# Kernel optimization log

Measured on AMD Instinct MI355X. Metric: run time of the kernel, lower is better.

The kernel has to match this reference:

```python
import jax, jax.numpy as jnp
import numpy as np

D_MODEL = 2048
EXPAND = 2
D_INNER = D_MODEL * EXPAND            # 4096
HEAD_DIM = 64
NHEADS = D_INNER // HEAD_DIM          # 64
D_STATE = 128
NGROUPS = 1
D_CONV = 4
CHUNK = 256
CONV_DIM = D_INNER + 2 * NGROUPS * D_STATE      # 4352
D_IN_PROJ = 2 * D_INNER + 2 * NGROUPS * D_STATE + NHEADS  # 8512
EPS = 1e-5


def segsum(x):
    # x: [..., T] -> [..., T, T] lower-triangular segment sums (incl. diagonal)
    T = x.shape[-1]
    xc = jnp.cumsum(x, axis=-1)
    diff = xc[..., :, None] - xc[..., None, :]
    mask = jnp.tril(jnp.ones((T, T), dtype=bool))
    return jnp.where(mask, diff, -jnp.inf)


def causal_conv1d(x, w, b):
    # x: [B,L,C]  depthwise causal conv, kernel K; w: [C,K], b: [C]
    K = w.shape[1]
    L = x.shape[1]
    xp = jnp.pad(x, ((0, 0), (K - 1, 0), (0, 0)))
    y = b[None, None, :]
    for k in range(K):
        y = y + xp[:, k:k + L, :] * w[None, None, :, k]
    return jax.nn.silu(y)


def ssd_chunked(x, dt, A, B, C, Dskip):
    # x:[b,l,h,p] dt:[b,l,h] A:[h] B,C:[b,l,g,n] Dskip:[h]
    b, l, h, p = x.shape
    g, n = B.shape[2], B.shape[3]
    c = l // CHUNK
    xc = x.reshape(b, c, CHUNK, h, p)
    dtc = dt.reshape(b, c, CHUNK, h)
    Bh = jnp.repeat(B.reshape(b, c, CHUNK, g, n), h // g, axis=3)  # [b,c,s,h,n]
    Ch = jnp.repeat(C.reshape(b, c, CHUNK, g, n), h // g, axis=3)
    dA = dtc * A[None, None, None, :]            # [b,c,s,h]
    dAc = jnp.moveaxis(dA, 3, 1)                 # [b,h,c,s]
    A_cumsum = jnp.cumsum(dAc, axis=-1)          # [b,h,c,s]
    Lmat = jnp.exp(segsum(dAc))                  # [b,h,c,s,s]
    # intra-chunk (diagonal blocks)
    Y_diag = jnp.einsum('bclhn,bcshn,bhcls,bcsh,bcshp->bclhp', Ch, Bh, Lmat, dtc, xc)
    # per-chunk final states
    decay_states = jnp.exp(A_cumsum[..., -1:] - A_cumsum)   # [b,h,c,s]
    states = jnp.einsum('bclhn,bhcl,bclh,bclhp->bchpn', Bh, decay_states, dtc, xc)
    states = jnp.concatenate([jnp.zeros_like(states[:, :1]), states], axis=1)  # [b,c+1,h,p,n]
    # inter-chunk recurrence
    chunk_sums = jnp.pad(A_cumsum[..., -1], ((0, 0), (0, 0), (1, 0)))  # [b,h,c+1]
    decay_chunk = jnp.exp(segsum(chunk_sums))    # [b,h,c+1,c+1]
    new_states = jnp.einsum('bhzc,bchpn->bzhpn', decay_chunk, states)
    states_prev = new_states[:, :-1]             # state entering each chunk
    state_decay_out = jnp.exp(A_cumsum)          # [b,h,c,s]
    Y_off = jnp.einsum('bclhn,bchpn,bhcl->bclhp', Ch, states_prev, state_decay_out)
    Y = (Y_diag + Y_off).reshape(b, l, h, p) + x * Dskip[None, None, :, None]
    return Y


def gated_rmsnorm(y, z, w):
    # norm_before_gate=False: rmsnorm(y * silu(z)) * w, grouped (g=NGROUPS)
    x = y * jax.nn.silu(z)
    gs = D_INNER // NGROUPS
    xg = x.reshape(x.shape[:-1] + (NGROUPS, gs))
    var = jnp.mean(xg * xg, axis=-1, keepdims=True)
    xg = xg * jax.lax.rsqrt(var + EPS)
    return xg.reshape(x.shape) * w[None, None, :]


def setup_inputs() -> dict:
    key = jax.random.key(0)
    ks = jax.random.split(key, 9)
    B, L = 2, 2048
    return {
        'hidden_states': jax.random.normal(ks[0], (B, L, D_MODEL), jnp.float32),
        'W_in': jax.random.normal(ks[1], (D_MODEL, D_IN_PROJ), jnp.float32) * 0.02,
        'conv_w': jax.random.normal(ks[2], (CONV_DIM, D_CONV), jnp.float32) * 0.2,
        'conv_b': jax.random.normal(ks[3], (CONV_DIM,), jnp.float32) * 0.02,
        'A': -jnp.exp(jax.random.normal(ks[4], (NHEADS,), jnp.float32) * 0.5),
        'D': jax.random.normal(ks[5], (NHEADS,), jnp.float32) * 0.5,
        'dt_bias': jax.random.normal(ks[6], (NHEADS,), jnp.float32) * 0.5,
        'norm_w': jnp.ones((D_INNER,), jnp.float32) + jax.random.normal(ks[7], (D_INNER,), jnp.float32) * 0.02,
        'W_out': jax.random.normal(ks[8], (D_INNER, D_MODEL), jnp.float32) * 0.02,
    }


def reference(hidden_states, W_in, conv_w, conv_b, A, D, dt_bias, norm_w, W_out):
    b, l, _ = hidden_states.shape
    zxbcdt = hidden_states @ W_in  # [b,l,d_in_proj]
    z = zxbcdt[..., :D_INNER]
    xbc = zxbcdt[..., D_INNER:D_INNER + CONV_DIM]
    dt = zxbcdt[..., D_INNER + CONV_DIM:]
    xbc = causal_conv1d(xbc, conv_w, conv_b)
    x = xbc[..., :D_INNER].reshape(b, l, NHEADS, HEAD_DIM)
    Bs = xbc[..., D_INNER:D_INNER + NGROUPS * D_STATE].reshape(b, l, NGROUPS, D_STATE)
    Cs = xbc[..., D_INNER + NGROUPS * D_STATE:].reshape(b, l, NGROUPS, D_STATE)
    dt = jax.nn.softplus(dt + dt_bias[None, None, :])
    y = ssd_chunked(x, dt, A, Bs, Cs, D).reshape(b, l, D_INNER)
    y = gated_rmsnorm(y, z, norm_w)
    return y @ W_out
```

## Files before the change

kernel.cpp:

```cpp
#include <hip/hip_runtime.h>
#include <hip/hip_bf16.h>
#include <math.h>

#define D_MODEL   2048
#define D_INNER   4096
#define NHEADS    64
#define HEAD_DIM  64
#define D_STATE   128
#define CHUNK     256
#define CONV_DIM  (D_INNER + 2*D_STATE)
#define D_IN_PROJ (2*D_INNER + 2*D_STATE + NHEADS)
#define LD_ZX     8704
#define DT_OFF    (2*D_INNER + 2*D_STATE)
#define BATCH     2
#define SEQ       2048
#define NCHUNK    (SEQ/CHUNK)
#define EPS_RMS   1e-5f
#define MROWS     4096
#define TSTRIDE   ((size_t)MROWS * 512)

typedef unsigned short u16;
typedef __attribute__((ext_vector_type(8))) unsigned short u16x8;
typedef __attribute__((ext_vector_type(4))) unsigned short u16x4;
typedef __attribute__((ext_vector_type(8))) short bf16x8;
typedef __attribute__((ext_vector_type(4))) float f32x4;

__device__ __forceinline__ float us2f(u16 u){
    union { unsigned int i; float f; } c; c.i = ((unsigned int)u) << 16; return c.f;
}
__device__ __forceinline__ u16 f2us(float f){
    union { float f; unsigned int i; } c; c.f = f;
    unsigned int r = c.i + 0x7FFFu + ((c.i >> 16) & 1u);
    return (u16)(r >> 16);
}
__device__ __forceinline__ float siluf(float x){ return x / (1.f + expf(-x)); }

__device__ __forceinline__ void gload_lds16(const void* g, void* l) {
    __builtin_amdgcn_global_load_lds((const __attribute__((address_space(1))) void*)g,
                                     (__attribute__((address_space(3))) void*)l, 16, 0, 0);
}

#define VMCNT(n) asm volatile("s_waitcnt vmcnt(" #n ")" ::: "memory")

__device__ __forceinline__ void stage_half(const u16* __restrict__ g, size_t ldk,
                                           u16* ldsbase, int w, int lane)
{
    #pragma unroll
    for (int cc = 0; cc < 2; cc++) {
        int cb = cc * 512 + w * 64;
        int ci = cb + lane;
        int sc = ci ^ ((ci >> 3) & 7);
        gload_lds16(&g[(size_t)(sc >> 3) * ldk + (sc & 7) * 8], ldsbase + cb * 8);
    }
}

__global__ __launch_bounds__(256)
void cvt_bf16(const float* __restrict__ in, u16* __restrict__ out, int n4)
{
    int i = blockIdx.x * 256 + threadIdx.x;
    if (i >= n4) return;
    float4 v = *(const float4*)&in[(size_t)i * 4];
    u16x4 o; o[0]=f2us(v.x); o[1]=f2us(v.y); o[2]=f2us(v.z); o[3]=f2us(v.w);
    *(u16x4*)&out[(size_t)i * 4] = o;
}

__global__ __launch_bounds__(256)
void add_tmp_bf16(float* __restrict__ out, const u16* __restrict__ tmp, int n8)
{
    int i = blockIdx.x * 256 + threadIdx.x;
    if (i >= n8) return;
    u16x8 b = *(const u16x8*)&tmp[(size_t)i * 8];
    float* o = &out[(size_t)i * 8];
    float4 a0 = *(const float4*)&o[0];
    float4 a1 = *(const float4*)&o[4];
    *(float4*)&o[0] = make_float4(a0.x+us2f(b[0]), a0.y+us2f(b[1]), a0.z+us2f(b[2]), a0.w+us2f(b[3]));
    *(float4*)&o[4] = make_float4(a1.x+us2f(b[4]), a1.y+us2f(b[5]), a1.z+us2f(b[6]), a1.w+us2f(b[7]));
}

__global__ __launch_bounds__(256)
void transpose_cvt(const float* __restrict__ in, u16* __restrict__ out, int K, int N)
{
    __shared__ u16 tile[64][65];
    int k0 = blockIdx.x * 64;
    int n0 = blockIdx.y * 64;
    int t = threadIdx.x;
    #pragma unroll
    for (int q = 0; q < 16; q++) {
        int lin = q * 256 + t;
        int r = lin >> 6, c = lin & 63;
        int n = n0 + c;
        float v = (n < N) ? in[(size_t)(k0 + r) * N + n] : 0.f;
        tile[r][c] = f2us(v);
    }
    __syncthreads();
    #pragma unroll
    for (int q = 0; q < 4; q++) {
        int lin = q * 256 + t;
        int r = lin >> 4, cg = lin & 15;
        u16x4 v;
        #pragma unroll
        for (int e = 0; e < 4; e++) v[e] = tile[cg*4 + e][r];
        *(u16x4*)&out[(size_t)(n0 + r) * K + k0 + cg*4] = v;
    }
}

template<typename TC, bool KSPLIT>
__global__ __launch_bounds__(512, 1)
void gemm_8ph(const u16* __restrict__ Ag, const u16* __restrict__ Btg,
              TC* __restrict__ Cg, u16* __restrict__ Cg2,
              int M, int N, int Kext, int ldk, int ldc)
{
    __shared__ u16 smA[2][2][8192];
    __shared__ u16 smB[2][2][8192];
    const int tid = threadIdx.x;
    const int lane = tid & 63, w = tid >> 6;
    const int wm = w >> 2, wn = w & 3;
    const int lr = lane & 15, kh = lane >> 4;
    const int swz = (lr & 7) << 3;

    int orig = blockIdx.x;
    int ntile = gridDim.x;
    int kidx = 0;
    if constexpr (KSPLIT) { kidx = orig & 1; orig >>= 1; ntile >>= 1; }

    const int nbx = N >> 8;
    const int qq = ntile >> 3, r8 = ntile & 7;
    const int xcd = orig & 7, loc = orig >> 3;
    const int wgid = (xcd < r8 ? xcd*(qq+1) : r8*(qq+1) + (xcd-r8)*qq) + loc;
    const int m0 = (wgid / nbx) * 256;
    const int n0 = (wgid % nbx) * 256;

    if constexpr (KSPLIT) {
        Ag  += (size_t)kidx * Kext;
        Btg += (size_t)kidx * Kext;
    }
    const int NT = Kext >> 6;

    f32x4 acc[8][4];
    #pragma unroll
    for (int i = 0; i < 8; i++)
        #pragma unroll
        for (int j = 0; j < 4; j++) acc[i][j] = (f32x4){0.f,0.f,0.f,0.f};

    stage_half(&Ag [(size_t)(m0      ) * ldk      ], ldk, &smA[0][0][0], w, lane);
    stage_half(&Ag [(size_t)(m0 + 128) * ldk      ], ldk, &smA[0][1][0], w, lane);
    stage_half(&Btg[(size_t)(n0      ) * ldk      ], ldk, &smB[0][0][0], w, lane);
    stage_half(&Btg[(size_t)(n0 + 128) * ldk      ], ldk, &smB[0][1][0], w, lane);
    stage_half(&Ag [(size_t)(m0      ) * ldk + 64 ], ldk, &smA[1][0][0], w, lane);
    stage_half(&Btg[(size_t)(n0      ) * ldk + 64 ], ldk, &smB[1][0][0], w, lane);
    stage_half(&Btg[(size_t)(n0 + 128) * ldk + 64 ], ldk, &smB[1][1][0], w, lane);
    VMCNT(6);
    __builtin_amdgcn_s_barrier();

    for (int t = 0; t < NT; ++t) {
        const int d = t & 1;
        const u16* As = &smA[d][wm][0];
        const u16* Bs = &smB[d][wn >> 1][0];
        const int rb = (wn & 1) * 64;

        bf16x8 aF[4][2], bLo[2][2], bHi[2][2];

        #pragma unroll
        for (int i = 0; i < 4; i++)
            #pragma unroll
            for (int ks = 0; ks < 2; ks++)
                aF[i][ks] = *(const bf16x8*)&As[(i*16 + lr)*64 + ((ks*32 + kh*8) ^ swz)];
        #pragma unroll
        for (int j = 0; j < 2; j++)
            #pragma unroll
            for (int ks = 0; ks < 2; ks++)
                bLo[j][ks] = *(const bf16x8*)&Bs[(rb + j*16 + lr)*64 + ((ks*32 + kh*8) ^ swz)];
        if (t + 1 < NT)
            stage_half(&Ag[(size_t)(m0 + 128) * ldk + (t+1)*64], ldk, &smA[d^1][1][0], w, lane);
        __builtin_amdgcn_s_barrier();
        __builtin_amdgcn_s_setprio(1);
        #pragma unroll
        for (int i = 0; i < 4; i++)
            #pragma unroll
            for (int j = 0; j < 2; j++)
                #pragma unroll
                for (int ks = 0; ks < 2; ks++)
                    acc[i][j] = __builtin_amdgcn_mfma_f32_16x16x32_bf16(aF[i][ks], bLo[j][ks], acc[i][j], 0, 0, 0);
        __builtin_amdgcn_s_setprio(0);
        __builtin_amdgcn_s_barrier();

        #pragma unroll
        for (int j = 0; j < 2; j++)
            #pragma unroll
            for (int ks = 0; ks < 2; ks++)
                bHi[j][ks] = *(const bf16x8*)&Bs[(rb + (2+j)*16 + lr)*64 + ((ks*32 + kh*8) ^ swz)];
        __builtin_amdgcn_s_barrier();
        __builtin_amdgcn_s_setprio(1);
        #pragma unroll
        for (int i = 0; i < 4; i++)
            #pragma unroll
            for (int j = 0; j < 2; j++)
                #pragma unroll
                for (int ks = 0; ks < 2; ks++)
                    acc[i][2+j] = __builtin_amdgcn_mfma_f32_16x16x32_bf16(aF[i][ks], bHi[j][ks], acc[i][2+j], 0, 0, 0);
        __builtin_amdgcn_s_setprio(0);
        __builtin_amdgcn_s_barrier();

        #pragma unroll
        for (int i = 0; i < 4; i++)
            #pragma unroll
            for (int ks = 0; ks < 2; ks++)
                aF[i][ks] = *(const bf16x8*)&As[(64 + i*16 + lr)*64 + ((ks*32 + kh*8) ^ swz)];
        if (t + 2 < NT)
            stage_half(&Btg[(size_t)(n0) * ldk + (t+2)*64], ldk, &smB[d][0][0], w, lane);
        __builtin_amdgcn_s_barrier();
        __builtin_amdgcn_s_setprio(1);
        #pragma unroll
        for (int i = 0; i < 4; i++)
            #pragma unroll
            for (int j = 0; j < 2; j++)
                #pragma unroll
                for (int ks = 0; ks < 2; ks++)
                    acc[4+i][j] = __builtin_amdgcn_mfma_f32_16x16x32_bf16(aF[i][ks], bLo[j][ks], acc[4+i][j], 0, 0, 0);
        __builtin_amdgcn_s_setprio(0);
        __builtin_amdgcn_s_barrier();

        if (t + 2 < NT) {
            stage_half(&Btg[(size_t)(n0 + 128) * ldk + (t+2)*64], ldk, &smB[d][1][0], w, lane);
            stage_half(&Ag [(size_t)(m0      ) * ldk + (t+2)*64], ldk, &smA[d][0][0], w, lane);
        }
        __builtin_amdgcn_s_barrier();
        __builtin_amdgcn_s_setprio(1);
        #pragma unroll
        for (int i = 0; i < 4; i++)
            #pragma unroll
            for (int j = 0; j < 2; j++)
                #pragma unroll
                for (int ks = 0; ks < 2; ks++)
                    acc[4+i][2+j] = __builtin_amdgcn_mfma_f32_16x16x32_bf16(aF[i][ks], bHi[j][ks], acc[4+i][2+j], 0, 0, 0);
        __builtin_amdgcn_s_setprio(0);
        if (t < NT - 2)       { VMCNT(6); }
        else if (t == NT - 2) { VMCNT(0); }
        __builtin_amdgcn_s_barrier();
    }

    #pragma unroll
    for (int mf = 0; mf < 8; mf++) {
        #pragma unroll
        for (int nf = 0; nf < 4; nf++) {
            int r = m0 + wm*128 + mf*16 + kh*4;
            int cidx = n0 + wn*64 + nf*16 + lr;
            #pragma unroll
            for (int q = 0; q < 4; q++) {
                if (KSPLIT && kidx) {
                    Cg2[(size_t)(r+q)*ldc + cidx] = f2us(acc[mf][nf][q]);
                } else if constexpr (sizeof(TC) == 4) {
                    Cg[(size_t)(r+q)*ldc + cidx] = acc[mf][nf][q];
                } else {
                    Cg[(size_t)(r+q)*ldc + cidx] = f2us(acc[mf][nf][q]);
                }
            }
        }
    }
}

__global__ __launch_bounds__(256)
void gemm_tail_ks4(const u16* __restrict__ A, const u16* __restrict__ Bt,
                   float* __restrict__ Cp, int M, int ldk)
{
    __shared__ u16 Asm[128][32];
    __shared__ u16 Bsm[128][32];
    const int t = threadIdx.x;
    const int lane = t & 63, w = t >> 6;
    const int wr = w >> 1, wc = w & 1;
    const int lr = lane & 15, kh = lane >> 4;

    const int bid = blockIdx.x;
    const int kidx = bid & 3, tile = bid >> 2;
    const int m0 = (tile >> 2) * 128;
    const int n0 = (tile & 3) * 128;

    const u16* Ak = A  + kidx * 512;
    const u16* Bk = Bt + kidx * 512;
    float* C = Cp + (size_t)kidx * TSTRIDE;

    f32x4 acc[4][4];
    #pragma unroll
    for (int i = 0; i < 4; i++)
        #pragma unroll
        for (int j = 0; j < 4; j++) acc[i][j] = (f32x4){0.f,0.f,0.f,0.f};

    for (int k0 = 0; k0 < 512; k0 += 32) {
        #pragma unroll
        for (int i = 0; i < 2; i++) {
            int cb = i * 256 + w * 64;
            int chunk = cb + lane;
            int row = chunk >> 2, kb = chunk & 3;
            gload_lds16(&Ak[(size_t)(m0 + row) * ldk + k0 + kb * 8], &Asm[0][0] + cb * 8);
            gload_lds16(&Bk[(size_t)(n0 + row) * ldk + k0 + kb * 8], &Bsm[0][0] + cb * 8);
        }
        __syncthreads();
        bf16x8 af[4], bf[4];
        #pragma unroll
        for (int i = 0; i < 4; i++)
            af[i] = *(const bf16x8*)&Asm[wr*64 + i*16 + lr][kh*8];
        #pragma unroll
        for (int j = 0; j < 4; j++)
            bf[j] = *(const bf16x8*)&Bsm[wc*64 + j*16 + lr][kh*8];
        #pragma unroll
        for (int i = 0; i < 4; i++)
            #pragma unroll
            for (int j = 0; j < 4; j++)
                acc[i][j] = __builtin_amdgcn_mfma_f32_16x16x32_bf16(af[i], bf[j], acc[i][j], 0, 0, 0);
        __syncthreads();
    }
    #pragma unroll
    for (int i = 0; i < 4; i++) {
        #pragma unroll
        for (int j = 0; j < 4; j++) {
            int r = m0 + wr*64 + i*16 + kh*4;
            int cidx = n0 + wc*64 + j*16 + lr;
            #pragma unroll
            for (int q = 0; q < 4; q++)
                C[(size_t)(r+q)*512 + cidx] = acc[i][j][q];
        }
    }
}

__global__ __launch_bounds__(256)
void conv_silu(const u16* __restrict__ zx, const float* __restrict__ tailp,
               const float* __restrict__ cw, const float* __restrict__ cb,
               u16* __restrict__ xconv, u16* __restrict__ Bbuf, u16* __restrict__ Cbuf)
{
    int idx = blockIdx.x * 256 + threadIdx.x;
    int cg = idx % (CONV_DIM / 8);
    int r  = idx / (CONV_DIM / 8);
    int c0 = cg * 8;
    int l  = r & (SEQ - 1);

    float y[8];
    {
        float4 b0 = *(const float4*)&cb[c0];
        float4 b1 = *(const float4*)&cb[c0 + 4];
        y[0]=b0.x; y[1]=b0.y; y[2]=b0.z; y[3]=b0.w;
        y[4]=b1.x; y[5]=b1.y; y[6]=b1.z; y[7]=b1.w;
    }
    float cwf[8][4];
    #pragma unroll
    for (int e = 0; e < 8; e++) {
        float4 v = *(const float4*)&cw[(c0 + e) * 4];
        cwf[e][0]=v.x; cwf[e][1]=v.y; cwf[e][2]=v.z; cwf[e][3]=v.w;
    }
    if (c0 < D_INNER) {
        #pragma unroll
        for (int k = 0; k < 4; k++) {
            if (l + k - 3 >= 0) {
                u16x8 v = *(const u16x8*)&zx[(size_t)(r + k - 3) * LD_ZX + D_INNER + c0];
                #pragma unroll
                for (int e = 0; e < 8; e++) y[e] += us2f(v[e]) * cwf[e][k];
            }
        }
    } else {
        int tc = c0 - D_INNER;
        #pragma unroll
        for (int k = 0; k < 4; k++) {
            if (l + k - 3 >= 0) {
                const float* tb = &tailp[(size_t)(r + k - 3) * 512 + tc];
                #pragma unroll
                for (int e = 0; e < 8; e++) {
                    float s = tb[e] + tb[TSTRIDE + e] + tb[2*TSTRIDE + e] + tb[3*TSTRIDE + e];
                    y[e] += s * cwf[e][k];
                }
            }
        }
    }
    u16x8 o;
    #pragma unroll
    for (int e = 0; e < 8; e++) {
        float s = y[e] / (1.f + expf(-y[e]));
        o[e] = f2us(s);
    }
    if (c0 < D_INNER)                *(u16x8*)&xconv[(size_t)r * D_INNER + c0] = o;
    else if (c0 < D_INNER + D_STATE) *(u16x8*)&Bbuf[(size_t)r * D_STATE + (c0 - D_INNER)] = o;
    else                             *(u16x8*)&Cbuf[(size_t)r * D_STATE + (c0 - D_INNER - D_STATE)] = o;
}

__global__ __launch_bounds__(256)
void dt_acs(const float* __restrict__ tailp, const float* __restrict__ Aparam,
            const float* __restrict__ dt_bias, float* __restrict__ dtT,
            float* __restrict__ Acs)
{
    __shared__ float sb[CHUNK];
    int blk = blockIdx.x;
    int c = blk & 7, h = (blk >> 3) & 63, b = blk >> 9;
    int t = threadIdx.x;
    int lg = c * CHUNK + t;
    int row = b * SEQ + lg;
    const float* tb = &tailp[(size_t)row * 512 + 256 + h];
    float x = tb[0] + tb[TSTRIDE] + tb[2*TSTRIDE] + tb[3*TSTRIDE];
    x += dt_bias[h];
    float dt = (x > 20.f) ? x : log1pf(expf(x));
    float v = dt * Aparam[h];
    sb[t] = v; __syncthreads();
    #pragma unroll
    for (int off = 1; off < 256; off <<= 1) {
        float add = (t >= off) ? sb[t - off] : 0.f;
        __syncthreads();
        v += add; sb[t] = v;
        __syncthreads();
    }
    int o = (b * NHEADS + h) * SEQ + lg;
    dtT[o] = dt;
    Acs[o] = v;
}

__global__ __launch_bounds__(256)
void chunk_states_mfma(const u16* __restrict__ xconv, const u16* __restrict__ Bbuf,
                       const float* __restrict__ dtT, const float* __restrict__ Acs,
                       u16* __restrict__ states)
{
    __shared__ u16 Btsh[128][72];
    __shared__ u16 xtsh[64][72];
    __shared__ float acs_sh[CHUNK];
    __shared__ float dt_sh[CHUNK];

    const int blk = blockIdx.x;
    const int h = blk & 63, c = (blk >> 6) & 7, b = blk >> 9;
    const int t = threadIdx.x;
    const int lane = t & 63, w = t >> 6;
    const int wr = w >> 1, wc = w & 1;
    const int lr = lane & 15, kh = lane >> 4;
    const int bh = b * NHEADS + h;
    const size_t rowbase = (size_t)(b * SEQ + c * CHUNK);

    acs_sh[t] = Acs[(size_t)bh * SEQ + c * CHUNK + t];
    dt_sh[t]  = dtT[(size_t)bh * SEQ + c * CHUNK + t];
    __syncthreads();
    const float acs_last = acs_sh[CHUNK - 1];

    f32x4 acc[4][2];
    #pragma unroll
    for (int j = 0; j < 4; j++)
        #pragma unroll
        for (int i = 0; i < 2; i++) acc[j][i] = (f32x4){0.f,0.f,0.f,0.f};

    for (int lt = 0; lt < 4; lt++) {
        __syncthreads();
        const int s = t & 63;
        const int sg = lt * 64 + s;
        const float wgt = dt_sh[sg] * expf(acs_last - acs_sh[sg]);
        {
            int ng = (t >> 6) * 32;
            const u16* src = &Bbuf[(rowbase + sg) * D_STATE + ng];
            #pragma unroll
            for (int q = 0; q < 4; q++) {
                u16x8 v = *(const u16x8*)&src[q * 8];
                #pragma unroll
                for (int e = 0; e < 8; e++)
                    Btsh[ng + q*8 + e][s] = v[e];
            }
        }
        {
            int pg = (t >> 6) * 16;
            const u16* src = &xconv[(rowbase + sg) * D_INNER + h * HEAD_DIM + pg];
            u16x8 v0 = *(const u16x8*)&src[0];
            u16x8 v1 = *(const u16x8*)&src[8];
            #pragma unroll
            for (int e = 0; e < 8; e++) {
                xtsh[pg + e][s]     = f2us(us2f(v0[e]) * wgt);
                xtsh[pg + 8 + e][s] = f2us(us2f(v1[e]) * wgt);
            }
        }
        __syncthreads();
        #pragma unroll
        for (int kk = 0; kk < 2; kk++) {
            bf16x8 xf[2], bf[4];
            #pragma unroll
            for (int i = 0; i < 2; i++)
                xf[i] = *(const bf16x8*)&xtsh[wr*32 + i*16 + lr][kk*32 + kh*8];
            #pragma unroll
            for (int j = 0; j < 4; j++)
                bf[j] = *(const bf16x8*)&Btsh[wc*64 + j*16 + lr][kk*32 + kh*8];
            #pragma unroll
            for (int j = 0; j < 4; j++)
                #pragma unroll
                for (int i = 0; i < 2; i++)
                    acc[j][i] = __builtin_amdgcn_mfma_f32_16x16x32_bf16(bf[j], xf[i], acc[j][i], 0, 0, 0);
        }
    }
    size_t base = ((size_t)((b*NCHUNK + c)*NHEADS + h)) * (HEAD_DIM * D_STATE);
    #pragma unroll
    for (int j = 0; j < 4; j++) {
        #pragma unroll
        for (int i = 0; i < 2; i++) {
            int p = wr*32 + i*16 + lr;
            int n = wc*64 + j*16 + kh*4;
            u16x4 o;
            #pragma unroll
            for (int q = 0; q < 4; q++) o[q] = f2us(acc[j][i][q]);
            *(u16x4*)&states[base + (size_t)p * D_STATE + n] = o;
        }
    }
}

__global__ __launch_bounds__(256)
void state_recurrence(u16* __restrict__ states, const float* __restrict__ Acs)
{
    int idx = blockIdx.x * 256 + threadIdx.x;
    int n8 = idx & 15;
    int p  = (idx >> 4) & 63;
    int bh = idx >> 10;
    int b = bh >> 6, h = bh & 63;
    float E[8];
    #pragma unroll
    for (int e = 0; e < 8; e++) E[e] = 0.f;
    for (int c = 0; c < NCHUNK; c++) {
        size_t off = ((size_t)((b*NCHUNK + c)*NHEADS + h)) * 8192 + (size_t)p * 128 + n8 * 8;
        u16x8 sv = *(const u16x8*)&states[off];
        u16x8 ev;
        #pragma unroll
        for (int e = 0; e < 8; e++) ev[e] = f2us(E[e]);
        *(u16x8*)&states[off] = ev;
        float g = expf(Acs[(size_t)(b*NHEADS + h) * SEQ + c*CHUNK + 255]);
        #pragma unroll
        for (int e = 0; e < 8; e++) E[e] = g * E[e] + us2f(sv[e]);
    }
}

__global__ __launch_bounds__(256, 1)
void chunk_output_mfma(const u16* __restrict__ xconv, const u16* __restrict__ Bbuf,
                       const u16* __restrict__ Cbuf, const float* __restrict__ dtT,
                       const float* __restrict__ Acs, const u16* __restrict__ states,
                       const float* __restrict__ Dparam, u16* __restrict__ Y)
{
    __shared__ u16 Bsm[64][136];
    __shared__ u16 xt[64][72];
    __shared__ u16 Pt[4][64][72];
    __shared__ float acs_sh[CHUNK];
    __shared__ float dt_sh[CHUNK];

    const int blk = blockIdx.x;
    const int h = blk & 63, c = (blk >> 6) & 7, b = blk >> 9;
    const int t = threadIdx.x;
    const int lane = t & 63, w = t >> 6;
    const int lr = lane & 15, kh = lane >> 4;
    const int bh = b * NHEADS + h;
    const size_t rowbase = (size_t)(b * SEQ + c * CHUNK);

    acs_sh[t] = Acs[(size_t)bh * SEQ + c * CHUNK + t];
    dt_sh[t]  = dtT[(size_t)bh * SEQ + c * CHUNK + t];

    bf16x8 af[4][4];
    #pragma unroll
    for (int i = 0; i < 4; i++)
        #pragma unroll
        for (int kk = 0; kk < 4; kk++)
            af[i][kk] = *(const bf16x8*)&Cbuf[(rowbase + w*64 + i*16 + lr) * D_STATE + kk*32 + kh*8];

    {
        int p = t >> 2, ng = (t & 3) * 32;
        const u16* src = &states[((size_t)((b*NCHUNK + c)*NHEADS + h)) * 8192 + (size_t)p * 128 + ng];
        #pragma unroll
        for (int q = 0; q < 4; q++)
            *(u16x8*)&Bsm[p][ng + q*8] = *(const u16x8*)&src[q*8];
    }
    __syncthreads();
    float acs_l[4], el[4];
    #pragma unroll
    for (int i = 0; i < 4; i++) { acs_l[i] = acs_sh[w*64 + i*16 + lr]; el[i] = expf(acs_l[i]); }

    f32x4 yacc[4][4];
    #pragma unroll
    for (int j = 0; j < 4; j++)
        #pragma unroll
        for (int i = 0; i < 4; i++) yacc[j][i] = (f32x4){0.f,0.f,0.f,0.f};
    #pragma unroll
    for (int kk = 0; kk < 4; kk++) {
        bf16x8 pvA[4];
        #pragma unroll
        for (int j = 0; j < 4; j++)
            pvA[j] = *(const bf16x8*)&Bsm[j*16 + lr][kk*32 + kh*8];
        #pragma unroll
        for (int j = 0; j < 4; j++)
            #pragma unroll
            for (int i = 0; i < 4; i++)
                yacc[j][i] = __builtin_amdgcn_mfma_f32_16x16x32_bf16(pvA[j], af[i][kk], yacc[j][i], 0, 0, 0);
    }
    #pragma unroll
    for (int j = 0; j < 4; j++)
        #pragma unroll
        for (int i = 0; i < 4; i++)
            #pragma unroll
            for (int q = 0; q < 4; q++)
                yacc[j][i][q] *= el[i];

    for (int st = 0; st < 4; st++) {
        __syncthreads();
        {
            int sr = t >> 2, cg = (t & 3) * 32;
            const u16* src = &Bbuf[(rowbase + st*64 + sr) * D_STATE + cg];
            #pragma unroll
            for (int q = 0; q < 4; q++)
                *(u16x8*)&Bsm[sr][cg + q*8] = *(const u16x8*)&src[q*8];
        }
        {
            int s = t & 63, pg = t >> 6;
            const u16* src = &xconv[(rowbase + st*64 + s) * D_INNER + h*HEAD_DIM + pg*16];
            u16x8 v0 = *(const u16x8*)&src[0];
            u16x8 v1 = *(const u16x8*)&src[8];
            #pragma unroll
            for (int q = 0; q < 8; q++) { xt[pg*16 + q][s] = v0[q]; xt[pg*16 + 8 + q][s] = v1[q]; }
        }
        __syncthreads();
        if (st > w) continue;

        f32x4 sacc[4][4];
        #pragma unroll
        for (int js = 0; js < 4; js++)
            #pragma unroll
            for (int i = 0; i < 4; i++) sacc[js][i] = (f32x4){0.f,0.f,0.f,0.f};
        #pragma unroll
        for (int kk = 0; kk < 4; kk++) {
            bf16x8 bA[4];
            #pragma unroll
            for (int js = 0; js < 4; js++)
                bA[js] = *(const bf16x8*)&Bsm[js*16 + lr][kk*32 + kh*8];
            #pragma unroll
            for (int js = 0; js < 4; js++)
                #pragma unroll
                for (int i = 0; i < 4; i++)
                    sacc[js][i] = __builtin_amdgcn_mfma_f32_16x16x32_bf16(bA[js], af[i][kk], sacc[js][i], 0, 0, 0);
        }
        #pragma unroll
        for (int js = 0; js < 4; js++) {
            int s0 = st*64 + js*16;
            float as0 = acs_sh[s0];
            int sgq = s0 + kh*4;
            float eneg[4];
            #pragma unroll
            for (int q = 0; q < 4; q++)
                eneg[q] = expf(fminf(as0 - acs_sh[sgq + q], 60.f)) * dt_sh[sgq + q];
            #pragma unroll
            for (int i = 0; i < 4; i++) {
                float eladj = expf(acs_l[i] - as0);
                int lg = w*64 + i*16 + lr;
                u16x4 pv;
                #pragma unroll
                for (int q = 0; q < 4; q++) {
                    float fac = (sgq + q <= lg) ? eladj * eneg[q] : 0.f;
                    pv[q] = f2us(sacc[js][i][q] * fac);
                }
                *(u16x4*)&Pt[w][i*16 + lr][js*16 + kh*4] = pv;
            }
        }
        #pragma unroll
        for (int kk2 = 0; kk2 < 2; kk2++) {
            bf16x8 xA[4], pB[4];
            #pragma unroll
            for (int j = 0; j < 4; j++)
                xA[j] = *(const bf16x8*)&xt[j*16 + lr][kk2*32 + kh*8];
            #pragma unroll
            for (int i = 0; i < 4; i++)
                pB[i] = *(const bf16x8*)&Pt[w][i*16 + lr][kk2*32 + kh*8];
            #pragma unroll
            for (int j = 0; j < 4; j++)
                #pragma unroll
                for (int i = 0; i < 4; i++)
                    yacc[j][i] = __builtin_amdgcn_mfma_f32_16x16x32_bf16(xA[j], pB[i], yacc[j][i], 0, 0, 0);
        }
    }

    float Dh = Dparam[h];
    #pragma unroll
    for (int i = 0; i < 4; i++) {
        #pragma unroll
        for (int j = 0; j < 4; j++) {
            size_t o = (rowbase + w*64 + i*16 + lr) * D_INNER + h*HEAD_DIM + j*16 + kh*4;
            u16x4 xv = *(const u16x4*)&xconv[o];
            u16x4 ov;
            #pragma unroll
            for (int q = 0; q < 4; q++)
                ov[q] = f2us(yacc[j][i][q] + Dh * us2f(xv[q]));
            *(u16x4*)&Y[o] = ov;
        }
    }
}

__global__ __launch_bounds__(256)
void gated_rmsnorm_k(u16* __restrict__ Y, const u16* __restrict__ zx,
                     const float* __restrict__ nw)
{
    __shared__ float xs[D_INNER];
    __shared__ float red[8];
    int row = blockIdx.x;
    int t = threadIdx.x;
    float ss = 0.f;
    for (int i = t*8; i < D_INNER; i += 2048) {
        u16x8 yv = *(const u16x8*)&Y[(size_t)row * D_INNER + i];
        u16x8 zv = *(const u16x8*)&zx[(size_t)row * LD_ZX + i];
        #pragma unroll
        for (int q = 0; q < 8; q++) {
            float x = us2f(yv[q]) * siluf(us2f(zv[q]));
            xs[i + q] = x;
            ss += x * x;
        }
    }
    #pragma unroll
    for (int off = 32; off > 0; off >>= 1) ss += __shfl_down(ss, off);
    int wid = t >> 6, lane = t & 63;
    if (lane == 0) red[wid] = ss;
    __syncthreads();
    if (t == 0) {
        float tot = red[0] + red[1] + red[2] + red[3];
        red[0] = rsqrtf(tot / (float)D_INNER + EPS_RMS);
    }
    __syncthreads();
    float sc = red[0];
    for (int i = t*8; i < D_INNER; i += 2048) {
        u16x8 o;
        #pragma unroll
        for (int q = 0; q < 8; q++) o[q] = f2us(xs[i + q] * sc * nw[i + q]);
        *(u16x8*)&Y[(size_t)row * D_INNER + i] = o;
    }
}

__global__ void ws_fail_k(float* out, float mb){ out[threadIdx.x] = mb; }

extern "C" void kernel_launch(void* const* d_in, const int* in_sizes, int n_in,
                              void* d_out, int out_size, void* d_ws, size_t ws_size,
                              hipStream_t stream)
{
    const float* hidden  = (const float*)d_in[0];
    const float* W_in    = (const float*)d_in[1];
    const float* conv_w  = (const float*)d_in[2];
    const float* conv_b  = (const float*)d_in[3];
    const float* Aparam  = (const float*)d_in[4];
    const float* Dparam  = (const float*)d_in[5];
    const float* dt_bias = (const float*)d_in[6];
    const float* norm_w  = (const float*)d_in[7];
    const float* W_out   = (const float*)d_in[8];
    float* out = (float*)d_out;

    const int M = BATCH * SEQ;

    size_t off = 0;
    char* wsb = (char*)d_ws;
    u16*   zx     = (u16*)  (wsb + off); off += (size_t)M * LD_ZX * 2;
    u16*   xconv  = (u16*)  (wsb + off); off += (size_t)M * D_INNER * 2;
    u16*   Bbuf   = (u16*)  (wsb + off); off += (size_t)M * D_STATE * 2;
    u16*   Cbuf   = (u16*)  (wsb + off); off += (size_t)M * D_STATE * 2;
    float* dtT    = (float*)(wsb + off); off += (size_t)BATCH * NHEADS * SEQ * 4;
    float* Acs    = (float*)(wsb + off); off += (size_t)BATCH * NHEADS * SEQ * 4;
    u16*   states = (u16*)  (wsb + off); off += (size_t)BATCH * NCHUNK * NHEADS * HEAD_DIM * D_STATE * 2;
    u16*   Ybuf   = (u16*)  (wsb + off); off += (size_t)M * D_INNER * 2;
    u16*   hbf    = (u16*)  (wsb + off); off += (size_t)M * D_MODEL * 2;
    u16*   WtIn   = (u16*)  (wsb + off); off += (size_t)LD_ZX * D_MODEL * 2;
    u16*   WtOut  = (u16*)  (wsb + off); off += (size_t)D_MODEL * D_INNER * 2;
    float* tailp  = (float*)(wsb + off); off += 4 * TSTRIDE * 4;
    u16*   tmpf   = (u16*)zx;

    if (off > ws_size) {
        ws_fail_k<<<1, 64, 0, stream>>>(out, (float)(ws_size >> 20));
        return;
    }

    cvt_bf16<<<(M * D_MODEL / 4 + 255) / 256, 256, 0, stream>>>(hidden, hbf, M * D_MODEL / 4);
    transpose_cvt<<<dim3(D_MODEL/64, LD_ZX/64), 256, 0, stream>>>(W_in, WtIn, D_MODEL, D_IN_PROJ);
    transpose_cvt<<<dim3(D_INNER/64, D_MODEL/64), 256, 0, stream>>>(W_out, WtOut, D_INNER, D_MODEL);

    gemm_8ph<u16, false><<<(8192/256) * (M/256), 512, 0, stream>>>(
        hbf, WtIn, zx, nullptr, M, 8192, D_MODEL, D_MODEL, LD_ZX);
    gemm_tail_ks4<<<512, 256, 0, stream>>>(hbf, WtIn + (size_t)8192 * D_MODEL, tailp, M, D_MODEL);

    conv_silu<<<(M * CONV_DIM / 8) / 256, 256, 0, stream>>>(zx, tailp, conv_w, conv_b, xconv, Bbuf, Cbuf);
    dt_acs<<<BATCH * NHEADS * NCHUNK, 256, 0, stream>>>(tailp, Aparam, dt_bias, dtT, Acs);
    chunk_states_mfma<<<BATCH * NCHUNK * NHEADS, 256, 0, stream>>>(xconv, Bbuf, dtT, Acs, states);
    state_recurrence<<<(BATCH * NHEADS * 64 * 16) / 256, 256, 0, stream>>>(states, Acs);
    chunk_output_mfma<<<BATCH * NCHUNK * NHEADS, 256, 0, stream>>>(xconv, Bbuf, Cbuf, dtT, Acs, states, Dparam, Ybuf);
    gated_rmsnorm_k<<<M, 256, 0, stream>>>(Ybuf, zx, norm_w);

    gemm_8ph<float, true><<<2 * (D_MODEL/256) * (M/256), 512, 0, stream>>>(
        Ybuf, WtOut, out, tmpf, M, D_MODEL, D_INNER/2, D_INNER, D_MODEL);
    add_tmp_bf16<<<(M * D_MODEL / 8 + 255) / 256, 256, 0, stream>>>(out, tmpf, M * D_MODEL / 8);
}
```

Measured before the change: 476.8 us.

## Precompute head-shared C·Bᵀ per chunk and write both split-K halves as bf16

With one group, the per-chunk C·Bᵀ score matrix is the same for every head. A new kernel computes the lower-triangular 64x64 blocks of it once per (batch, chunk) and stores them as bf16. The chunk output kernel then reads those scores instead of recomputing them with MFMA for each of the 64 heads. This removes redundant matmul work and B staging, at the cost of extra global reads and bf16 rounding of the scores. Separately, the split-K out-projection now writes both halves as bf16 temporaries that a final kernel sums, instead of writing fp32 output and then reading it back to add the second half.

```diff
diff --git a/kernel.cpp b/kernel.cpp
--- a/kernel.cpp
+++ b/kernel.cpp
@@ -65,16 +65,18 @@
 }
 
 __global__ __launch_bounds__(256)
-void add_tmp_bf16(float* __restrict__ out, const u16* __restrict__ tmp, int n8)
+void add2_bf16(float* __restrict__ out, const u16* __restrict__ t0,
+               const u16* __restrict__ t1, int n8)
 {
     int i = blockIdx.x * 256 + threadIdx.x;
     if (i >= n8) return;
-    u16x8 b = *(const u16x8*)&tmp[(size_t)i * 8];
+    u16x8 a = *(const u16x8*)&t0[(size_t)i * 8];
+    u16x8 b = *(const u16x8*)&t1[(size_t)i * 8];
     float* o = &out[(size_t)i * 8];
-    float4 a0 = *(const float4*)&o[0];
-    float4 a1 = *(const float4*)&o[4];
-    *(float4*)&o[0] = make_float4(a0.x+us2f(b[0]), a0.y+us2f(b[1]), a0.z+us2f(b[2]), a0.w+us2f(b[3]));
-    *(float4*)&o[4] = make_float4(a1.x+us2f(b[4]), a1.y+us2f(b[5]), a1.z+us2f(b[6]), a1.w+us2f(b[7]));
+    *(float4*)&o[0] = make_float4(us2f(a[0])+us2f(b[0]), us2f(a[1])+us2f(b[1]),
+                                  us2f(a[2])+us2f(b[2]), us2f(a[3])+us2f(b[3]));
+    *(float4*)&o[4] = make_float4(us2f(a[4])+us2f(b[4]), us2f(a[5])+us2f(b[5]),
+                                  us2f(a[6])+us2f(b[6]), us2f(a[7])+us2f(b[7]));
 }
 
 __global__ __launch_bounds__(256)
@@ -133,6 +135,7 @@
     if constexpr (KSPLIT) {
         Ag  += (size_t)kidx * Kext;
         Btg += (size_t)kidx * Kext;
+        Cg2 += (size_t)kidx * M * ldc;
     }
     const int NT = Kext >> 6;
 
@@ -247,7 +250,7 @@
             int cidx = n0 + wn*64 + nf*16 + lr;
             #pragma unroll
             for (int q = 0; q < 4; q++) {
-                if (KSPLIT && kidx) {
+                if constexpr (KSPLIT) {
                     Cg2[(size_t)(r+q)*ldc + cidx] = f2us(acc[mf][nf][q]);
                 } else if constexpr (sizeof(TC) == 4) {
                     Cg[(size_t)(r+q)*ldc + cidx] = acc[mf][nf][q];
@@ -410,6 +413,40 @@
 }
 
 __global__ __launch_bounds__(256)
+void s_precompute(const u16* __restrict__ Bbuf, const u16* __restrict__ Cbuf,
+                  u16* __restrict__ Sbuf)
+{
+    int p = blockIdx.x % 10, bc = blockIdx.x / 10;
+    int q = (p >= 6) ? 3 : (p >= 3) ? 2 : (p >= 1) ? 1 : 0;
+    int st = p - q * (q + 1) / 2;
+    int b = bc >> 3, c = bc & 7;
+    const int lane = threadIdx.x & 63, w = threadIdx.x >> 6;
+    const int lr = lane & 15, kh = lane >> 4;
+    const size_t rowbase = (size_t)(b * SEQ + c * CHUNK);
+
+    f32x4 sacc[4];
+    #pragma unroll
+    for (int i = 0; i < 4; i++) sacc[i] = (f32x4){0.f,0.f,0.f,0.f};
+    #pragma unroll
+    for (int kk = 0; kk < 4; kk++) {
+        bf16x8 bA = *(const bf16x8*)&Bbuf[(rowbase + st*64 + w*16 + lr) * D_STATE + kk*32 + kh*8];
+        #pragma unroll
+        for (int i = 0; i < 4; i++) {
+            bf16x8 af = *(const bf16x8*)&Cbuf[(rowbase + q*64 + i*16 + lr) * D_STATE + kk*32 + kh*8];
+            sacc[i] = __builtin_amdgcn_mfma_f32_16x16x32_bf16(bA, af, sacc[i], 0, 0, 0);
+        }
+    }
+    u16* Sb = Sbuf + (size_t)bc * 256 * 256;
+    #pragma unroll
+    for (int i = 0; i < 4; i++) {
+        u16x4 o;
+        #pragma unroll
+        for (int qq = 0; qq < 4; qq++) o[qq] = f2us(sacc[i][qq]);
+        *(u16x4*)&Sb[(size_t)(q*64 + i*16 + lr) * 256 + st*64 + w*16 + kh*4] = o;
+    }
+}
+
+__global__ __launch_bounds__(256)
 void chunk_states_mfma(const u16* __restrict__ xconv, const u16* __restrict__ Bbuf,
                        const float* __restrict__ dtT, const float* __restrict__ Acs,
                        u16* __restrict__ states)
@@ -523,7 +560,7 @@
 }
 
 __global__ __launch_bounds__(256, 1)
-void chunk_output_mfma(const u16* __restrict__ xconv, const u16* __restrict__ Bbuf,
+void chunk_output_mfma(const u16* __restrict__ xconv, const u16* __restrict__ Sbuf,
                        const u16* __restrict__ Cbuf, const float* __restrict__ dtT,
                        const float* __restrict__ Acs, const u16* __restrict__ states,
                        const float* __restrict__ Dparam, u16* __restrict__ Y)
@@ -541,6 +578,7 @@
     const int lr = lane & 15, kh = lane >> 4;
     const int bh = b * NHEADS + h;
     const size_t rowbase = (size_t)(b * SEQ + c * CHUNK);
+    const u16* Sblk = Sbuf + (size_t)(b * NCHUNK + c) * 256 * 256;
 
     acs_sh[t] = Acs[(size_t)bh * SEQ + c * CHUNK + t];
     dt_sh[t]  = dtT[(size_t)bh * SEQ + c * CHUNK + t];
@@ -591,13 +629,6 @@
 
     for (int st = 0; st < 4; st++) {
         __syncthreads();
-        {
-            int sr = t >> 2, cg = (t & 3) * 32;
-            const u16* src = &Bbuf[(rowbase + st*64 + sr) * D_STATE + cg];
-            #pragma unroll
-            for (int q = 0; q < 4; q++)
-                *(u16x8*)&Bsm[sr][cg + q*8] = *(const u16x8*)&src[q*8];
-        }
         {
             int s = t & 63, pg = t >> 6;
             const u16* src = &xconv[(rowbase + st*64 + s) * D_INNER + h*HEAD_DIM + pg*16];
@@ -609,23 +640,6 @@
         __syncthreads();
         if (st > w) continue;
 
-        f32x4 sacc[4][4];
-        #pragma unroll
-        for (int js = 0; js < 4; js++)
-            #pragma unroll
-            for (int i = 0; i < 4; i++) sacc[js][i] = (f32x4){0.f,0.f,0.f,0.f};
-        #pragma unroll
-        for (int kk = 0; kk < 4; kk++) {
-            bf16x8 bA[4];
-            #pragma unroll
-            for (int js = 0; js < 4; js++)
-                bA[js] = *(const bf16x8*)&Bsm[js*16 + lr][kk*32 + kh*8];
-            #pragma unroll
-            for (int js = 0; js < 4; js++)
-                #pragma unroll
-                for (int i = 0; i < 4; i++)
-                    sacc[js][i] = __builtin_amdgcn_mfma_f32_16x16x32_bf16(bA[js], af[i][kk], sacc[js][i], 0, 0, 0);
-        }
         #pragma unroll
         for (int js = 0; js < 4; js++) {
             int s0 = st*64 + js*16;
@@ -637,13 +651,14 @@
                 eneg[q] = expf(fminf(as0 - acs_sh[sgq + q], 60.f)) * dt_sh[sgq + q];
             #pragma unroll
             for (int i = 0; i < 4; i++) {
+                int ll = w*64 + i*16 + lr;
                 float eladj = expf(acs_l[i] - as0);
-                int lg = w*64 + i*16 + lr;
+                u16x4 sv = *(const u16x4*)&Sblk[(size_t)ll * 256 + sgq];
                 u16x4 pv;
                 #pragma unroll
                 for (int q = 0; q < 4; q++) {
-                    float fac = (sgq + q <= lg) ? eladj * eneg[q] : 0.f;
-                    pv[q] = f2us(sacc[js][i][q] * fac);
+                    float fac = (sgq + q <= ll) ? eladj * eneg[q] : 0.f;
+                    pv[q] = f2us(us2f(sv[q]) * fac);
                 }
                 *(u16x4*)&Pt[w][i*16 + lr][js*16 + kh*4] = pv;
             }
@@ -752,6 +767,7 @@
     u16*   WtIn   = (u16*)  (wsb + off); off += (size_t)LD_ZX * D_MODEL * 2;
     u16*   WtOut  = (u16*)  (wsb + off); off += (size_t)D_MODEL * D_INNER * 2;
     float* tailp  = (float*)(wsb + off); off += 4 * TSTRIDE * 4;
+    u16*   Sbuf   = (u16*)  (wsb + off); off += (size_t)16 * 256 * 256 * 2;
     u16*   tmpf   = (u16*)zx;
 
     if (off > ws_size) {
@@ -768,13 +784,15 @@
     gemm_tail_ks4<<<512, 256, 0, stream>>>(hbf, WtIn + (size_t)8192 * D_MODEL, tailp, M, D_MODEL);
 
     conv_silu<<<(M * CONV_DIM / 8) / 256, 256, 0, stream>>>(zx, tailp, conv_w, conv_b, xconv, Bbuf, Cbuf);
+    s_precompute<<<160, 256, 0, stream>>>(Bbuf, Cbuf, Sbuf);
     dt_acs<<<BATCH * NHEADS * NCHUNK, 256, 0, stream>>>(tailp, Aparam, dt_bias, dtT, Acs);
     chunk_states_mfma<<<BATCH * NCHUNK * NHEADS, 256, 0, stream>>>(xconv, Bbuf, dtT, Acs, states);
     state_recurrence<<<(BATCH * NHEADS * 64 * 16) / 256, 256, 0, stream>>>(states, Acs);
-    chunk_output_mfma<<<BATCH * NCHUNK * NHEADS, 256, 0, stream>>>(xconv, Bbuf, Cbuf, dtT, Acs, states, Dparam, Ybuf);
+    chunk_output_mfma<<<BATCH * NCHUNK * NHEADS, 256, 0, stream>>>(xconv, Sbuf, Cbuf, dtT, Acs, states, Dparam, Ybuf);
     gated_rmsnorm_k<<<M, 256, 0, stream>>>(Ybuf, zx, norm_w);
 
     gemm_8ph<float, true><<<2 * (D_MODEL/256) * (M/256), 512, 0, stream>>>(
         Ybuf, WtOut, out, tmpf, M, D_MODEL, D_INNER/2, D_INNER, D_MODEL);
-    add_tmp_bf16<<<(M * D_MODEL / 8 + 255) / 256, 256, 0, stream>>>(out, tmpf, M * D_MODEL / 8);
-}
+    add2_bf16<<<(M * D_MODEL / 8 + 255) / 256, 256, 0, stream>>>(
+        out, tmpf, tmpf + (size_t)M * D_MODEL, M * D_MODEL / 8);
+}
```

After: 466.9 us. 2.1% less time.
